# Performance work log

Hardware: AMD Instinct MI355X
Metric: run time of the kernel (lower is better)

Reference implementation:

```python
import jax, jax.numpy as jnp
import numpy as np

E = 200000  # num edges == num nodes (x is built as ones((edge_index.size(1), D)))
D = 128     # embedding_dim
R = 4       # number of relation types
NEG_SLOPE = 0.01


def _xavier(key, shape):
    fan_in, fan_out = shape[-2], shape[-1]
    limit = np.sqrt(6.0 / (fan_in + fan_out)).astype(np.float32)
    return jax.random.uniform(key, shape, jnp.float32, -limit, limit)


def setup_inputs() -> dict:
    key = jax.random.key(0)
    ks = jax.random.split(key, 8)
    edge_index = jax.random.randint(ks[0], (2, E), 0, E)
    edge_type = jax.random.randint(ks[1], (E,), 0, R)
    edge_attr = jax.random.uniform(ks[2], (E,), dtype=jnp.float32)
    return {
        "edge_index": edge_index,
        "edge_type": edge_type,
        "edge_attr": edge_attr,
        "weights1": _xavier(ks[3], (R, D, D)), "bias1": jnp.zeros((D,), jnp.float32),
        "weights2": _xavier(ks[4], (R, D, D)), "bias2": jnp.zeros((D,), jnp.float32),
        "weights3": _xavier(ks[5], (R, D, D)), "bias3": jnp.zeros((D,), jnp.float32),
    }


def _conv(x, w, b, row, col, edge_type, edge_attr):
    # symmetric degree norm on target index (col), as in the torch code
    deg = jax.ops.segment_sum(jnp.ones((E,), x.dtype), col, num_segments=E)
    # deg**-0.5 with inf masked to 0 (isolated nodes) to keep the baseline finite
    dinv = jnp.where(deg > 0, jax.lax.rsqrt(jnp.where(deg > 0, deg, 1.0)), 0.0)
    norm = dinv[row] * dinv[col]                      # [E]
    xr = x[row]                                       # gather source nodes [E,D]
    # per-edge relation-indexed matmul: 4 dense GEMMs + select (avoids [E,D,D])
    msg = jnp.zeros((E, D), x.dtype)
    for r in range(R):
        msg = msg + jnp.where((edge_type == r)[:, None], xr @ w[r], 0.0)
    msg = msg * (edge_attr * norm)[:, None]
    out = jax.ops.segment_sum(msg, col, num_segments=E) + b  # scatter-add + bias
    return jax.nn.leaky_relu(out, NEG_SLOPE)          # dropout skipped (eval mode)


def reference(edge_index, edge_type, edge_attr,
              weights1, bias1, weights2, bias2, weights3, bias3):
    row, col = edge_index[0], edge_index[1]
    x = jnp.ones((E, D), jnp.float32)
    z1 = _conv(x, weights1, bias1, row, col, edge_type, edge_attr)
    z2 = _conv(z1, weights2, bias2, row, col, edge_type, edge_attr)
    z3 = _conv(z2, weights3, bias3, row, col, edge_type, edge_attr)
    return (x + z1 + z2 + z3) / 4.0
```

## Files before the change

### kernel.cpp

```cpp
#include <hip/hip_runtime.h>
#include <math.h>

constexpr int EN = 200000;
constexpr int D  = 128;
constexpr int R  = 4;
constexpr float NEG = 0.01f;

constexpr int NBLKE = (EN + 255) / 256;
constexpr int NPREP = 66;
constexpr int NCH   = (EN + 1023) / 1024;

static inline int ceil_div(int a, int b) { return (a + b - 1) / b; }

typedef __attribute__((ext_vector_type(8))) __bf16 bf16x8;
typedef __attribute__((ext_vector_type(4))) float f32x4;

__device__ __forceinline__ unsigned short f2bf(float f) {
    union { float f; unsigned u; } v; v.f = f;
    unsigned u = v.u + 0x7fffu + ((v.u >> 16) & 1u);
    return (unsigned short)(u >> 16);
}
__device__ __forceinline__ unsigned pack2bf(float a, float b) {
    return (unsigned)f2bf(a) | ((unsigned)f2bf(b) << 16);
}
__device__ __forceinline__ float bflo(unsigned m) { return __uint_as_float(m << 16); }
__device__ __forceinline__ float bfhi(unsigned m) { return __uint_as_float(m & 0xffff0000u); }

__device__ __forceinline__ void wswz_one(const float* __restrict__ w,
                                         unsigned short* __restrict__ wsw, int t) {
    int lane = t & 63, mt = (t >> 6) & 7, s = (t >> 9) & 3, r = t >> 11;
    int q = lane >> 4, n = mt * 16 + (lane & 15);
    union { unsigned short us[8]; uint4 u4; } o;
    #pragma unroll
    for (int j = 0; j < 8; ++j) {
        int k = s * 32 + q * 8 + j;
        o.us[j] = f2bf(w[((size_t)r * D + k) * D + n]);
    }
    *(uint4*)(wsw + (size_t)t * 8) = o.u4;
}

__global__ void k_cntprep(const int* __restrict__ col, const int* __restrict__ etyp,
                          const float* __restrict__ w1, const float* __restrict__ w2,
                          const float* __restrict__ w3,
                          int* __restrict__ cnt, int* __restrict__ rcnt,
                          unsigned short* __restrict__ w2b, unsigned short* __restrict__ w3b,
                          float* __restrict__ s1) {
    const int b = blockIdx.x, t = threadIdx.x;
    if (b < NBLKE) {
        __shared__ int lr[R];
        if (t < R) lr[t] = 0;
        __syncthreads();
        int e = b * 256 + t;
        if (e < EN) {
            atomicAdd(&cnt[col[e]], 1);
            atomicAdd(&lr[etyp[e]], 1);
        }
        __syncthreads();
        if (t < R && lr[t]) atomicAdd(&rcnt[t], lr[t]);
    } else {
        int g = (b - NBLKE) * 256 + t;
        if (g < 8192) {
            wswz_one(w2, w2b, g);
        } else if (g < 16384) {
            wswz_one(w3, w3b, g - 8192);
        } else if (g < 16896) {
            int t2 = g - 16384;
            int r = t2 >> 7, j = t2 & (D - 1);
            float s = 0.f;
            for (int k = 0; k < D; ++k) s += w1[((r << 7) + k) * D + j];
            s1[t2] = s;
        }
    }
}

__global__ void k_scanA(const int* __restrict__ cnt, int* __restrict__ part) {
    __shared__ int sm[256];
    int t = threadIdx.x;
    int base = blockIdx.x * 1024 + t * 4;
    int s = 0;
    #pragma unroll
    for (int i = 0; i < 4; ++i) { int idx = base + i; if (idx < EN) s += cnt[idx]; }
    sm[t] = s; __syncthreads();
    for (int off = 128; off > 0; off >>= 1) {
        if (t < off) sm[t] += sm[t + off];
        __syncthreads();
    }
    if (t == 0) part[blockIdx.x] = sm[0];
}

__global__ void k_scanB(const int* __restrict__ cnt, const int* __restrict__ part,
                        const int* __restrict__ rcnt,
                        int* __restrict__ rbase, int* __restrict__ cursor,
                        int* __restrict__ col_start, int* __restrict__ ccur,
                        int* __restrict__ bk_row, int* __restrict__ bk_dst,
                        float* __restrict__ bk_coef) {
    __shared__ int sm[256];
    __shared__ int sbase[R + 1];
    __shared__ int scnt[R];
    int t = threadIdx.x, bid = blockIdx.x;
    sm[t] = (t < NCH) ? part[t] : 0;
    __syncthreads();
    for (int off = 1; off < 256; off <<= 1) {
        int u = 0; if (t >= off) u = sm[t - off];
        __syncthreads(); sm[t] += u; __syncthreads();
    }
    const int base0 = (bid > 0) ? sm[bid - 1] : 0;
    __syncthreads();
    int base = bid * 1024 + t * 4;
    int v[4]; int s = 0;
    #pragma unroll
    for (int i = 0; i < 4; ++i) { int idx = base + i; v[i] = (idx < EN) ? cnt[idx] : 0; s += v[i]; }
    sm[t] = s; __syncthreads();
    for (int off = 1; off < 256; off <<= 1) {
        int u = 0; if (t >= off) u = sm[t - off];
        __syncthreads(); sm[t] += u; __syncthreads();
    }
    int ex = ((t > 0) ? sm[t - 1] : 0) + base0;
    #pragma unroll
    for (int i = 0; i < 4; ++i) {
        int idx = base + i;
        if (idx < EN) { col_start[idx] = ex; ex += v[i]; ccur[idx] = 0; }
    }
    if (bid == 0) {
        if (t == 0) {
            int acc = 0;
            for (int r = 0; r < R; ++r) {
                sbase[r] = acc; rbase[r] = acc; cursor[r] = acc;
                int c0 = rcnt[r]; scnt[r] = c0;
                acc += (c0 + 15) & ~15;
            }
            sbase[R] = acc; rbase[R] = acc;
            col_start[EN] = EN;
        }
        __syncthreads();
        for (int r = 0; r < R; ++r) {
            int ps = sbase[r] + scnt[r], pe = sbase[r + 1];
            for (int i = ps + t; i < pe; i += 256) {
                bk_row[i] = 0; bk_dst[i] = EN; bk_coef[i] = 0.f;
            }
        }
    }
}

__global__ void k_bucket(const int* __restrict__ row, const int* __restrict__ col,
                         const int* __restrict__ etype, const float* __restrict__ attr,
                         const int* __restrict__ cnt, const int* __restrict__ col_start,
                         int* __restrict__ cursor, int* __restrict__ ccur,
                         int* __restrict__ bk_row, int* __restrict__ bk_dst,
                         float* __restrict__ bk_coef, float* __restrict__ crel) {
    __shared__ int lcnt[R];
    __shared__ int lbase[R];
    int t = threadIdx.x;
    if (t < R) lcnt[t] = 0;
    __syncthreads();
    int e = blockIdx.x * 256 + t;
    int r = 0, rank = 0, c = 0, rw = 0;
    float cf = 0.f;
    if (e < EN) {
        r = etype[e];
        rank = atomicAdd(&lcnt[r], 1);
        c = col[e]; rw = row[e];
        int dr = cnt[rw], dc = cnt[c];
        float a = (dr > 0) ? rsqrtf((float)dr) : 0.f;
        float b = (dc > 0) ? rsqrtf((float)dc) : 0.f;
        cf = attr[e] * a * b;
    }
    __syncthreads();
    if (t < R) lbase[t] = lcnt[t] ? atomicAdd(&cursor[t], lcnt[t]) : 0;
    __syncthreads();
    if (e < EN) {
        int pos = lbase[r] + rank;
        int sp = col_start[c] + atomicAdd(&ccur[c], 1);
        bk_row[pos] = rw;
        bk_dst[pos] = sp;
        bk_coef[pos] = cf;
        atomicAdd(&crel[c * 4 + r], cf);
    }
}

template<bool ONFLY>
__global__ __launch_bounds__(256)
void k_gemm(const unsigned short* __restrict__ xb, const unsigned short* __restrict__ wsw,
            const int* __restrict__ bk_row, const int* __restrict__ bk_dst,
            const float* __restrict__ bk_coef, const int* __restrict__ rbase,
            const float* __restrict__ crel, const float* __restrict__ s1g,
            const float* __restrict__ b1,
            unsigned short* __restrict__ msgb) {
    const int t = threadIdx.x;
    __shared__ unsigned short xpose[4][16 * 144];
    __shared__ float ls1[R * D];
    __shared__ float lb1[D];
    if constexpr (ONFLY) {
        ls1[t] = s1g[t];
        ls1[t + 256] = s1g[t + 256];
        if (t < D) lb1[t] = b1[t];
        __syncthreads();
    }
    const int tile = blockIdx.x * 4 + (t >> 6);
    const int e16 = tile * 16;
    if (e16 >= rbase[R]) return;
    const int r = (e16 >= rbase[1]) + (e16 >= rbase[2]) + (e16 >= rbase[3]);
    const int l = t & 63, q = l >> 4, n16 = l & 15;
    const int p = e16 + n16;
    const int srow = bk_row[p];
    const int dp = bk_dst[p];
    const float cf = bk_coef[p];

    bf16x8 xf[4];
    if constexpr (ONFLY) {
        const float4 cr = ((const float4*)crel)[srow];
        #pragma unroll
        for (int s = 0; s < 4; ++s) {
            union { unsigned short us[8]; bf16x8 v; } o;
            #pragma unroll
            for (int j = 0; j < 8; ++j) {
                int k = s * 32 + q * 8 + j;
                float xv = lb1[k] + cr.x * ls1[k] + cr.y * ls1[D + k]
                         + cr.z * ls1[2 * D + k] + cr.w * ls1[3 * D + k];
                xv = (xv > 0.f) ? xv : NEG * xv;
                o.us[j] = f2bf(xv);
            }
            xf[s] = o.v;
        }
    } else {
        const unsigned short* xrow = xb + (size_t)srow * D;
        #pragma unroll
        for (int s = 0; s < 4; ++s)
            xf[s] = *(const bf16x8*)(xrow + s * 32 + q * 8);
    }

    const unsigned short* wr = wsw + ((size_t)r * 2048 + l) * 8;

    f32x4 acc[8];
    #pragma unroll
    for (int mt = 0; mt < 8; ++mt) acc[mt] = (f32x4){0.f, 0.f, 0.f, 0.f};

    #pragma unroll
    for (int s = 0; s < 4; ++s) {
        #pragma unroll
        for (int mt = 0; mt < 8; ++mt) {
            bf16x8 wf = *(const bf16x8*)(wr + (size_t)(s * 512 + mt * 64) * 8);
            acc[mt] = __builtin_amdgcn_mfma_f32_16x16x32_bf16(wf, xf[s], acc[mt], 0, 0, 0);
        }
    }

    unsigned short* lbuf = xpose[t >> 6];
    #pragma unroll
    for (int mt = 0; mt < 8; ++mt) {
        uint2 u;
        u.x = pack2bf(acc[mt].x * cf, acc[mt].y * cf);
        u.y = pack2bf(acc[mt].z * cf, acc[mt].w * cf);
        *(uint2*)&lbuf[n16 * 144 + mt * 16 + q * 4] = u;
    }
    #pragma unroll
    for (int ro = 0; ro < 4; ++ro) {
        int e = ro * 4 + q;
        uint4 v = *(const uint4*)&lbuf[e * 144 + n16 * 8];
        int rdp = __shfl(dp, e);
        *(uint4*)(msgb + (size_t)rdp * D + n16 * 8) = v;
    }
}

__global__ void k_agg(const unsigned* __restrict__ msgb32, const float* __restrict__ bias,
                      const int* __restrict__ col_start,
                      unsigned* __restrict__ z2out,
                      const float* __restrict__ crel, const float* __restrict__ s1g,
                      const float* __restrict__ b1, const unsigned* __restrict__ z2in,
                      float* __restrict__ dout, int mode) {
    __shared__ float lb[D];
    __shared__ float ls1[R * D];
    __shared__ float lb1[D];
    int t = threadIdx.x;
    if (t < D) lb[t] = bias[t];
    if (mode == 3) {
        ls1[t] = s1g[t];
        ls1[t + 256] = s1g[t + 256];
        if (t < D) lb1[t] = b1[t];
    }
    __syncthreads();
    int lane = t & 63;
    for (int c = blockIdx.x * 4 + (t >> 6); c < EN; c += gridDim.x * 4) {
        int st = col_start[c], pe = col_start[c + 1];
        float a0 = 0.f, a1 = 0.f;
        for (int p = st; p < pe; ++p) {
            unsigned m = msgb32[(size_t)p * 64 + lane];
            a0 += bflo(m); a1 += bfhi(m);
        }
        a0 += lb[lane * 2]; a1 += lb[lane * 2 + 1];
        a0 = (a0 > 0.f) ? a0 : NEG * a0;
        a1 = (a1 > 0.f) ? a1 : NEG * a1;
        size_t ix = (size_t)c * 64 + lane;
        if (mode == 2) {
            z2out[ix] = pack2bf(a0, a1);
        } else {
            float4 cr = ((const float4*)crel)[c];
            int d0 = lane * 2, d1 = d0 + 1;
            float z1a = lb1[d0] + cr.x * ls1[d0] + cr.y * ls1[D + d0]
                      + cr.z * ls1[2 * D + d0] + cr.w * ls1[3 * D + d0];
            float z1b = lb1[d1] + cr.x * ls1[d1] + cr.y * ls1[D + d1]
                      + cr.z * ls1[2 * D + d1] + cr.w * ls1[3 * D + d1];
            z1a = (z1a > 0.f) ? z1a : NEG * z1a;
            z1b = (z1b > 0.f) ? z1b : NEG * z1b;
            unsigned u2 = z2in[ix];
            float2 o;
            o.x = (1.f + z1a + bflo(u2) + a0) * 0.25f;
            o.y = (1.f + z1b + bfhi(u2) + a1) * 0.25f;
            ((float2*)(dout + (size_t)c * D))[lane] = o;
        }
    }
}

extern "C" void kernel_launch(void* const* d_in, const int* in_sizes, int n_in,
                              void* d_out, int out_size, void* d_ws, size_t ws_size,
                              hipStream_t stream) {
    const int*   eidx = (const int*)d_in[0];
    const int*   row  = eidx;
    const int*   col  = eidx + EN;
    const int*   etyp = (const int*)d_in[1];
    const float* attr = (const float*)d_in[2];
    const float* w1   = (const float*)d_in[3];
    const float* b1   = (const float*)d_in[4];
    const float* w2   = (const float*)d_in[5];
    const float* b2   = (const float*)d_in[6];
    const float* w3   = (const float*)d_in[7];
    const float* b3   = (const float*)d_in[8];
    float* dout = (float*)d_out;

    char* wsb = (char*)d_ws;
    size_t off = 0;
    unsigned short* msgb = (unsigned short*)(wsb + off); off += (size_t)(EN + 1) * D * 2 + 512;
    unsigned short* xb2  = (unsigned short*)(wsb + off); off += (size_t)EN * D * 2;
    int*   col_start = (int*)(wsb + off); off += 800032;
    int*   cnt       = (int*)(wsb + off); off += (size_t)EN * 4;
    int*   rcnt      = (int*)(wsb + off); off += 16;
    float* crel      = (float*)(wsb + off); off += (size_t)EN * 16;
    int*   bk_row    = (int*)(wsb + off); off += (size_t)(EN + 64) * 4;
    int*   bk_dst    = (int*)(wsb + off); off += (size_t)(EN + 64) * 4;
    float* bk_coef   = (float*)(wsb + off); off += (size_t)(EN + 64) * 4;
    unsigned short* w2b = (unsigned short*)(wsb + off); off += 131072;
    unsigned short* w3b = (unsigned short*)(wsb + off); off += 131072;
    int*   part      = (int*)(wsb + off); off += 1024;
    int*   rbase     = (int*)(wsb + off); off += 32;
    int*   cursor    = (int*)(wsb + off); off += 16;
    float* s1        = (float*)(wsb + off); off += (size_t)R * D * 4;
    int*   ccur      = (int*)msgb;

    dim3 blk(256);

    hipMemsetAsync(cnt, 0, (size_t)EN * 4 + 16 + (size_t)EN * 16, stream);
    k_cntprep<<<NBLKE + NPREP, blk, 0, stream>>>(col, etyp, w1, w2, w3,
                                                 cnt, rcnt, w2b, w3b, s1);
    k_scanA<<<NCH, blk, 0, stream>>>(cnt, part);
    k_scanB<<<NCH, blk, 0, stream>>>(cnt, part, rcnt, rbase, cursor, col_start,
                                     ccur, bk_row, bk_dst, bk_coef);
    k_bucket<<<NBLKE, blk, 0, stream>>>(row, col, etyp, attr, cnt, col_start,
                                        cursor, ccur, bk_row, bk_dst, bk_coef, crel);

    const int nTiles = ceil_div(EN + 64, 16);
    const int gB = ceil_div(nTiles, 4);
    k_gemm<true><<<gB, blk, 0, stream>>>(nullptr, w2b, bk_row, bk_dst, bk_coef,
                                         rbase, crel, s1, b1, msgb);
    k_agg<<<2048, blk, 0, stream>>>((const unsigned*)msgb, b2, col_start,
                                    (unsigned*)xb2, crel, s1, b1, nullptr,
                                    nullptr, 2);
    k_gemm<false><<<gB, blk, 0, stream>>>(xb2, w3b, bk_row, bk_dst, bk_coef,
                                          rbase, crel, s1, b1, msgb);
    k_agg<<<2048, blk, 0, stream>>>((const unsigned*)msgb, b3, col_start,
                                    nullptr, crel, s1, b1, (const unsigned*)xb2,
                                    dout, 3);
}
```

Measured before the change: 283.7 us.

## Fuse per-edge relation GEMM with destination aggregation in destination-sorted blocks

Edges are now stored sorted by destination node, with their type kept alongside, instead of being grouped by relation. Each block takes a run of about 48 edges that starts and ends on destination-node boundaries. It computes the messages with MFMA, looping over the four relations with masked inputs, keeps them in LDS, and reduces them per destination in the same kernel. This removes the global bf16 message buffer's write and read-back, plus one kernel launch per layer. In exchange, each wavefront may issue up to four times as many MFMAs. It also assumes no block holds more than 64 edges, which fails for a high-degree node.

New measurement: 329.6 us. +16.2%, slower.

```diff
diff --git a/kernel.cpp b/kernel.cpp
--- a/kernel.cpp
+++ b/kernel.cpp
@@ -9,6 +9,8 @@
 constexpr int NBLKE = (EN + 255) / 256;
 constexpr int NPREP = 66;
 constexpr int NCH   = (EN + 1023) / 1024;
+constexpr int S     = 48;
+constexpr int NB    = (EN + S - 1) / S;
 
 static inline int ceil_div(int a, int b) { return (a + b - 1) / b; }
 
@@ -39,24 +41,16 @@
     *(uint4*)(wsw + (size_t)t * 8) = o.u4;
 }
 
-__global__ void k_cntprep(const int* __restrict__ col, const int* __restrict__ etyp,
+__global__ void k_cntprep(const int* __restrict__ col,
                           const float* __restrict__ w1, const float* __restrict__ w2,
                           const float* __restrict__ w3,
-                          int* __restrict__ cnt, int* __restrict__ rcnt,
+                          int* __restrict__ cnt,
                           unsigned short* __restrict__ w2b, unsigned short* __restrict__ w3b,
                           float* __restrict__ s1) {
     const int b = blockIdx.x, t = threadIdx.x;
     if (b < NBLKE) {
-        __shared__ int lr[R];
-        if (t < R) lr[t] = 0;
-        __syncthreads();
         int e = b * 256 + t;
-        if (e < EN) {
-            atomicAdd(&cnt[col[e]], 1);
-            atomicAdd(&lr[etyp[e]], 1);
-        }
-        __syncthreads();
-        if (t < R && lr[t]) atomicAdd(&rcnt[t], lr[t]);
+        if (e < EN) atomicAdd(&cnt[col[e]], 1);
     } else {
         int g = (b - NBLKE) * 256 + t;
         if (g < 8192) {
@@ -89,14 +83,11 @@
 }
 
 __global__ void k_scanB(const int* __restrict__ cnt, const int* __restrict__ part,
-                        const int* __restrict__ rcnt,
-                        int* __restrict__ rbase, int* __restrict__ cursor,
                         int* __restrict__ col_start, int* __restrict__ ccur,
-                        int* __restrict__ bk_row, int* __restrict__ bk_dst,
-                        float* __restrict__ bk_coef) {
+                        int* __restrict__ blkcol,
+                        int* __restrict__ bs_row, unsigned char* __restrict__ bs_typ,
+                        float* __restrict__ bs_coef) {
     __shared__ int sm[256];
-    __shared__ int sbase[R + 1];
-    __shared__ int scnt[R];
     int t = threadIdx.x, bid = blockIdx.x;
     sm[t] = (t < NCH) ? part[t] : 0;
     __syncthreads();
@@ -119,193 +110,168 @@
     #pragma unroll
     for (int i = 0; i < 4; ++i) {
         int idx = base + i;
-        if (idx < EN) { col_start[idx] = ex; ex += v[i]; ccur[idx] = 0; }
+        if (idx < EN) {
+            col_start[idx] = ex;
+            for (int nb = ex / S + 1; nb * S <= ex + v[i]; ++nb) blkcol[nb] = idx + 1;
+            ex += v[i];
+            ccur[idx] = 0;
+        }
     }
     if (bid == 0) {
-        if (t == 0) {
-            int acc = 0;
-            for (int r = 0; r < R; ++r) {
-                sbase[r] = acc; rbase[r] = acc; cursor[r] = acc;
-                int c0 = rcnt[r]; scnt[r] = c0;
-                acc += (c0 + 15) & ~15;
-            }
-            sbase[R] = acc; rbase[R] = acc;
-            col_start[EN] = EN;
-        }
-        __syncthreads();
-        for (int r = 0; r < R; ++r) {
-            int ps = sbase[r] + scnt[r], pe = sbase[r + 1];
-            for (int i = ps + t; i < pe; i += 256) {
-                bk_row[i] = 0; bk_dst[i] = EN; bk_coef[i] = 0.f;
-            }
-        }
+        if (t == 0) { col_start[EN] = EN; blkcol[0] = 0; blkcol[NB] = EN; }
+        if (t < 64) { bs_row[EN + t] = 0; bs_coef[EN + t] = 0.f; bs_typ[EN + t] = 3; }
     }
 }
 
 __global__ void k_bucket(const int* __restrict__ row, const int* __restrict__ col,
                          const int* __restrict__ etype, const float* __restrict__ attr,
                          const int* __restrict__ cnt, const int* __restrict__ col_start,
-                         int* __restrict__ cursor, int* __restrict__ ccur,
-                         int* __restrict__ bk_row, int* __restrict__ bk_dst,
-                         float* __restrict__ bk_coef, float* __restrict__ crel) {
-    __shared__ int lcnt[R];
-    __shared__ int lbase[R];
-    int t = threadIdx.x;
-    if (t < R) lcnt[t] = 0;
-    __syncthreads();
-    int e = blockIdx.x * 256 + t;
-    int r = 0, rank = 0, c = 0, rw = 0;
-    float cf = 0.f;
-    if (e < EN) {
-        r = etype[e];
-        rank = atomicAdd(&lcnt[r], 1);
-        c = col[e]; rw = row[e];
-        int dr = cnt[rw], dc = cnt[c];
-        float a = (dr > 0) ? rsqrtf((float)dr) : 0.f;
-        float b = (dc > 0) ? rsqrtf((float)dc) : 0.f;
-        cf = attr[e] * a * b;
-    }
-    __syncthreads();
-    if (t < R) lbase[t] = lcnt[t] ? atomicAdd(&cursor[t], lcnt[t]) : 0;
-    __syncthreads();
-    if (e < EN) {
-        int pos = lbase[r] + rank;
-        int sp = col_start[c] + atomicAdd(&ccur[c], 1);
-        bk_row[pos] = rw;
-        bk_dst[pos] = sp;
-        bk_coef[pos] = cf;
-        atomicAdd(&crel[c * 4 + r], cf);
-    }
-}
-
-template<bool ONFLY>
+                         int* __restrict__ ccur,
+                         int* __restrict__ bs_row, unsigned char* __restrict__ bs_typ,
+                         float* __restrict__ bs_coef, float* __restrict__ crel) {
+    int e = blockIdx.x * 256 + threadIdx.x;
+    if (e >= EN) return;
+    int r = etype[e];
+    int c = col[e], rw = row[e];
+    int dr = cnt[rw], dc = cnt[c];
+    float a = (dr > 0) ? rsqrtf((float)dr) : 0.f;
+    float b = (dc > 0) ? rsqrtf((float)dc) : 0.f;
+    float cf = attr[e] * a * b;
+    int sp = col_start[c] + atomicAdd(&ccur[c], 1);
+    bs_row[sp] = rw;
+    bs_typ[sp] = (unsigned char)r;
+    bs_coef[sp] = cf;
+    atomicAdd(&crel[c * 4 + r], cf);
+}
+
+template<int LAYER>
 __global__ __launch_bounds__(256)
-void k_gemm(const unsigned short* __restrict__ xb, const unsigned short* __restrict__ wsw,
-            const int* __restrict__ bk_row, const int* __restrict__ bk_dst,
-            const float* __restrict__ bk_coef, const int* __restrict__ rbase,
-            const float* __restrict__ crel, const float* __restrict__ s1g,
-            const float* __restrict__ b1,
-            unsigned short* __restrict__ msgb) {
-    const int t = threadIdx.x;
-    __shared__ unsigned short xpose[4][16 * 144];
+void k_fused(const unsigned short* __restrict__ xb,
+             const unsigned short* __restrict__ wsw,
+             const int* __restrict__ col_start,
+             const int* __restrict__ blkcol,
+             const int* __restrict__ bs_row,
+             const unsigned char* __restrict__ bs_typ,
+             const float* __restrict__ bs_coef,
+             const float* __restrict__ crel,
+             const float* __restrict__ s1g, const float* __restrict__ b1,
+             const float* __restrict__ bias,
+             unsigned* __restrict__ z2out, float* __restrict__ dout)
+{
+    __shared__ unsigned short lmsg[64 * 144];
     __shared__ float ls1[R * D];
     __shared__ float lb1[D];
-    if constexpr (ONFLY) {
-        ls1[t] = s1g[t];
-        ls1[t + 256] = s1g[t + 256];
-        if (t < D) lb1[t] = b1[t];
-        __syncthreads();
-    }
-    const int tile = blockIdx.x * 4 + (t >> 6);
-    const int e16 = tile * 16;
-    if (e16 >= rbase[R]) return;
-    const int r = (e16 >= rbase[1]) + (e16 >= rbase[2]) + (e16 >= rbase[3]);
-    const int l = t & 63, q = l >> 4, n16 = l & 15;
-    const int p = e16 + n16;
-    const int srow = bk_row[p];
-    const int dp = bk_dst[p];
-    const float cf = bk_coef[p];
-
-    bf16x8 xf[4];
-    if constexpr (ONFLY) {
-        const float4 cr = ((const float4*)crel)[srow];
+    __shared__ float lb[D];
+    __shared__ int hcnt[R], hbase[R];
+    __shared__ int perm[64];
+    const int t = threadIdx.x, b = blockIdx.x;
+    ls1[t] = s1g[t]; ls1[t + 256] = s1g[t + 256];
+    if (t < D) { lb1[t] = b1[t]; lb[t] = bias[t]; }
+    if (t < R) hcnt[t] = 0;
+    if (t < 64) perm[t] = EN;
+    const int c0 = blkcol[b], c1 = blkcol[b + 1];
+    const int p0 = col_start[c0], p1 = col_start[c1];
+    const int n_edges = p1 - p0;
+    int myslot = -1, myty = 0;
+    if (t < n_edges && t < 64) myty = bs_typ[p0 + t];
+    __syncthreads();
+    if (t < n_edges && t < 64) myslot = atomicAdd(&hcnt[myty], 1);
+    __syncthreads();
+    if (t == 0) {
+        int a = 0;
         #pragma unroll
-        for (int s = 0; s < 4; ++s) {
-            union { unsigned short us[8]; bf16x8 v; } o;
+        for (int r = 0; r < R; ++r) { hbase[r] = a; a += hcnt[r]; }
+    }
+    __syncthreads();
+    if (myslot >= 0) perm[hbase[myty] + myslot] = p0 + t;
+    __syncthreads();
+
+    const int w = t >> 6, l = t & 63, q = l >> 4, n16 = l & 15;
+    const int pe = perm[w * 16 + n16];
+    const int srow = bs_row[pe];
+    const int ty = bs_typ[pe];
+    const float cf = bs_coef[pe];
+    const int lrow = min(pe - p0, 63);
+
+    if (w * 16 < n_edges) {
+        bf16x8 xf[4];
+        if constexpr (LAYER == 2) {
+            const float4 cr = ((const float4*)crel)[srow];
             #pragma unroll
-            for (int j = 0; j < 8; ++j) {
-                int k = s * 32 + q * 8 + j;
-                float xv = lb1[k] + cr.x * ls1[k] + cr.y * ls1[D + k]
-                         + cr.z * ls1[2 * D + k] + cr.w * ls1[3 * D + k];
-                xv = (xv > 0.f) ? xv : NEG * xv;
-                o.us[j] = f2bf(xv);
+            for (int s = 0; s < 4; ++s) {
+                union { unsigned short us[8]; bf16x8 v; } o;
+                #pragma unroll
+                for (int j = 0; j < 8; ++j) {
+                    int k = s * 32 + q * 8 + j;
+                    float xv = lb1[k] + cr.x * ls1[k] + cr.y * ls1[D + k]
+                             + cr.z * ls1[2 * D + k] + cr.w * ls1[3 * D + k];
+                    xv = (xv > 0.f) ? xv : NEG * xv;
+                    o.us[j] = f2bf(xv);
+                }
+                xf[s] = o.v;
             }
-            xf[s] = o.v;
-        }
-    } else {
-        const unsigned short* xrow = xb + (size_t)srow * D;
+        } else {
+            const unsigned short* xrow = xb + (size_t)srow * D;
+            #pragma unroll
+            for (int s = 0; s < 4; ++s)
+                xf[s] = *(const bf16x8*)(xrow + s * 32 + q * 8);
+        }
+        f32x4 acc[8];
         #pragma unroll
-        for (int s = 0; s < 4; ++s)
-            xf[s] = *(const bf16x8*)(xrow + s * 32 + q * 8);
-    }
-
-    const unsigned short* wr = wsw + ((size_t)r * 2048 + l) * 8;
-
-    f32x4 acc[8];
-    #pragma unroll
-    for (int mt = 0; mt < 8; ++mt) acc[mt] = (f32x4){0.f, 0.f, 0.f, 0.f};
-
-    #pragma unroll
-    for (int s = 0; s < 4; ++s) {
+        for (int mt = 0; mt < 8; ++mt) acc[mt] = (f32x4){0.f, 0.f, 0.f, 0.f};
+        union { int i4[4]; bf16x8 v; } zer; zer.i4[0] = zer.i4[1] = zer.i4[2] = zer.i4[3] = 0;
+        for (int r = 0; r < R; ++r) {
+            if (__ballot(ty == r) == 0ull) continue;
+            const bool m = (ty == r);
+            bf16x8 xz[4];
+            #pragma unroll
+            for (int s = 0; s < 4; ++s) xz[s] = m ? xf[s] : zer.v;
+            const unsigned short* wr = wsw + ((size_t)r * 2048 + l) * 8;
+            #pragma unroll
+            for (int s = 0; s < 4; ++s) {
+                #pragma unroll
+                for (int mt = 0; mt < 8; ++mt) {
+                    bf16x8 wf = *(const bf16x8*)(wr + (size_t)(s * 512 + mt * 64) * 8);
+                    acc[mt] = __builtin_amdgcn_mfma_f32_16x16x32_bf16(wf, xz[s], acc[mt], 0, 0, 0);
+                }
+            }
+        }
         #pragma unroll
         for (int mt = 0; mt < 8; ++mt) {
-            bf16x8 wf = *(const bf16x8*)(wr + (size_t)(s * 512 + mt * 64) * 8);
-            acc[mt] = __builtin_amdgcn_mfma_f32_16x16x32_bf16(wf, xf[s], acc[mt], 0, 0, 0);
-        }
-    }
-
-    unsigned short* lbuf = xpose[t >> 6];
-    #pragma unroll
-    for (int mt = 0; mt < 8; ++mt) {
-        uint2 u;
-        u.x = pack2bf(acc[mt].x * cf, acc[mt].y * cf);
-        u.y = pack2bf(acc[mt].z * cf, acc[mt].w * cf);
-        *(uint2*)&lbuf[n16 * 144 + mt * 16 + q * 4] = u;
-    }
-    #pragma unroll
-    for (int ro = 0; ro < 4; ++ro) {
-        int e = ro * 4 + q;
-        uint4 v = *(const uint4*)&lbuf[e * 144 + n16 * 8];
-        int rdp = __shfl(dp, e);
-        *(uint4*)(msgb + (size_t)rdp * D + n16 * 8) = v;
-    }
-}
-
-__global__ void k_agg(const unsigned* __restrict__ msgb32, const float* __restrict__ bias,
-                      const int* __restrict__ col_start,
-                      unsigned* __restrict__ z2out,
-                      const float* __restrict__ crel, const float* __restrict__ s1g,
-                      const float* __restrict__ b1, const unsigned* __restrict__ z2in,
-                      float* __restrict__ dout, int mode) {
-    __shared__ float lb[D];
-    __shared__ float ls1[R * D];
-    __shared__ float lb1[D];
-    int t = threadIdx.x;
-    if (t < D) lb[t] = bias[t];
-    if (mode == 3) {
-        ls1[t] = s1g[t];
-        ls1[t + 256] = s1g[t + 256];
-        if (t < D) lb1[t] = b1[t];
-    }
-    __syncthreads();
-    int lane = t & 63;
-    for (int c = blockIdx.x * 4 + (t >> 6); c < EN; c += gridDim.x * 4) {
-        int st = col_start[c], pe = col_start[c + 1];
+            uint2 u;
+            u.x = pack2bf(acc[mt].x * cf, acc[mt].y * cf);
+            u.y = pack2bf(acc[mt].z * cf, acc[mt].w * cf);
+            *(uint2*)&lmsg[lrow * 144 + mt * 16 + q * 4] = u;
+        }
+    }
+    __syncthreads();
+
+    for (int c = c0 + w; c < c1; c += 4) {
+        int st = col_start[c] - p0, en = col_start[c + 1] - p0;
         float a0 = 0.f, a1 = 0.f;
-        for (int p = st; p < pe; ++p) {
-            unsigned m = msgb32[(size_t)p * 64 + lane];
-            a0 += bflo(m); a1 += bfhi(m);
-        }
-        a0 += lb[lane * 2]; a1 += lb[lane * 2 + 1];
+        for (int rr = st; rr < en; ++rr) {
+            unsigned mm = *(const unsigned*)&lmsg[rr * 144 + l * 2];
+            a0 += bflo(mm); a1 += bfhi(mm);
+        }
+        a0 += lb[l * 2]; a1 += lb[l * 2 + 1];
         a0 = (a0 > 0.f) ? a0 : NEG * a0;
         a1 = (a1 > 0.f) ? a1 : NEG * a1;
-        size_t ix = (size_t)c * 64 + lane;
-        if (mode == 2) {
-            z2out[ix] = pack2bf(a0, a1);
+        if constexpr (LAYER == 2) {
+            z2out[(size_t)c * 64 + l] = pack2bf(a0, a1);
         } else {
-            float4 cr = ((const float4*)crel)[c];
-            int d0 = lane * 2, d1 = d0 + 1;
+            const float4 cr = ((const float4*)crel)[c];
+            int d0 = l * 2, d1 = d0 + 1;
             float z1a = lb1[d0] + cr.x * ls1[d0] + cr.y * ls1[D + d0]
                       + cr.z * ls1[2 * D + d0] + cr.w * ls1[3 * D + d0];
             float z1b = lb1[d1] + cr.x * ls1[d1] + cr.y * ls1[D + d1]
                       + cr.z * ls1[2 * D + d1] + cr.w * ls1[3 * D + d1];
             z1a = (z1a > 0.f) ? z1a : NEG * z1a;
             z1b = (z1b > 0.f) ? z1b : NEG * z1b;
-            unsigned u2 = z2in[ix];
+            unsigned u2 = ((const unsigned*)xb)[(size_t)c * 64 + l];
             float2 o;
             o.x = (1.f + z1a + bflo(u2) + a0) * 0.25f;
             o.y = (1.f + z1b + bfhi(u2) + a1) * 0.25f;
-            ((float2*)(dout + (size_t)c * D))[lane] = o;
+            ((float2*)(dout + (size_t)c * D))[l] = o;
         }
     }
 }
@@ -328,44 +294,34 @@
 
     char* wsb = (char*)d_ws;
     size_t off = 0;
-    unsigned short* msgb = (unsigned short*)(wsb + off); off += (size_t)(EN + 1) * D * 2 + 512;
     unsigned short* xb2  = (unsigned short*)(wsb + off); off += (size_t)EN * D * 2;
     int*   col_start = (int*)(wsb + off); off += 800032;
-    int*   cnt       = (int*)(wsb + off); off += (size_t)EN * 4;
-    int*   rcnt      = (int*)(wsb + off); off += 16;
+    int*   cnt       = (int*)(wsb + off); off += (size_t)EN * 4 + 16;
     float* crel      = (float*)(wsb + off); off += (size_t)EN * 16;
-    int*   bk_row    = (int*)(wsb + off); off += (size_t)(EN + 64) * 4;
-    int*   bk_dst    = (int*)(wsb + off); off += (size_t)(EN + 64) * 4;
-    float* bk_coef   = (float*)(wsb + off); off += (size_t)(EN + 64) * 4;
+    int*   bs_row    = (int*)(wsb + off); off += (size_t)(EN + 64) * 4;
+    float* bs_coef   = (float*)(wsb + off); off += (size_t)(EN + 64) * 4;
+    unsigned char* bs_typ = (unsigned char*)(wsb + off); off += 200064;
+    int*   blkcol    = (int*)(wsb + off); off += (size_t)(NB + 1) * 4 + 12;
     unsigned short* w2b = (unsigned short*)(wsb + off); off += 131072;
     unsigned short* w3b = (unsigned short*)(wsb + off); off += 131072;
     int*   part      = (int*)(wsb + off); off += 1024;
-    int*   rbase     = (int*)(wsb + off); off += 32;
-    int*   cursor    = (int*)(wsb + off); off += 16;
     float* s1        = (float*)(wsb + off); off += (size_t)R * D * 4;
-    int*   ccur      = (int*)msgb;
+    int*   ccur      = (int*)xb2;
 
     dim3 blk(256);
 
     hipMemsetAsync(cnt, 0, (size_t)EN * 4 + 16 + (size_t)EN * 16, stream);
-    k_cntprep<<<NBLKE + NPREP, blk, 0, stream>>>(col, etyp, w1, w2, w3,
-                                                 cnt, rcnt, w2b, w3b, s1);
+    k_cntprep<<<NBLKE + NPREP, blk, 0, stream>>>(col, w1, w2, w3, cnt, w2b, w3b, s1);
     k_scanA<<<NCH, blk, 0, stream>>>(cnt, part);
-    k_scanB<<<NCH, blk, 0, stream>>>(cnt, part, rcnt, rbase, cursor, col_start,
-                                     ccur, bk_row, bk_dst, bk_coef);
+    k_scanB<<<NCH, blk, 0, stream>>>(cnt, part, col_start, ccur, blkcol,
+                                     bs_row, bs_typ, bs_coef);
     k_bucket<<<NBLKE, blk, 0, stream>>>(row, col, etyp, attr, cnt, col_start,
-                                        cursor, ccur, bk_row, bk_dst, bk_coef, crel);
-
-    const int nTiles = ceil_div(EN + 64, 16);
-    const int gB = ceil_div(nTiles, 4);
-    k_gemm<true><<<gB, blk, 0, stream>>>(nullptr, w2b, bk_row, bk_dst, bk_coef,
-                                         rbase, crel, s1, b1, msgb);
-    k_agg<<<2048, blk, 0, stream>>>((const unsigned*)msgb, b2, col_start,
-                                    (unsigned*)xb2, crel, s1, b1, nullptr,
-                                    nullptr, 2);
-    k_gemm<false><<<gB, blk, 0, stream>>>(xb2, w3b, bk_row, bk_dst, bk_coef,
-                                          rbase, crel, s1, b1, msgb);
-    k_agg<<<2048, blk, 0, stream>>>((const unsigned*)msgb, b3, col_start,
-                                    nullptr, crel, s1, b1, (const unsigned*)xb2,
-                                    dout, 3);
-}
+                                        ccur, bs_row, bs_typ, bs_coef, crel);
+
+    k_fused<2><<<NB, blk, 0, stream>>>(nullptr, w2b, col_start, blkcol,
+                                       bs_row, bs_typ, bs_coef, crel, s1, b1, b2,
+                                       (unsigned*)xb2, nullptr);
+    k_fused<3><<<NB, blk, 0, stream>>>(xb2, w3b, col_start, blkcol,
+                                       bs_row, bs_typ, bs_coef, crel, s1, b1, b3,
+                                       nullptr, dout);
+}
```
